# Performance work log

Hardware: AMD Instinct MI355X
Metric: run time of the kernel (lower is better)

Reference implementation:

```python
import jax, jax.numpy as jnp
import numpy as np

BN_EPS = 1e-5

def _bn_train(h, gamma, beta):
    # BatchNorm1d in training mode: batch statistics over the node dim
    mean = jnp.mean(h, axis=0)
    var = jnp.mean((h - mean) ** 2, axis=0)  # biased variance, as torch BN uses for normalization
    return gamma * (h - mean) * jax.lax.rsqrt(var + BN_EPS) + beta


def setup_inputs() -> dict:
    key = jax.random.key(0)
    ks = jax.random.split(key, 8)
    N, E = 100000, 1250000
    d_in, d_out = 64, 128
    x = jax.random.normal(ks[0], (N, d_in), dtype=jnp.float32)
    edge_index = jax.random.randint(ks[1], (2, E), 0, N, dtype=jnp.int64)
    s1 = 1.0 / np.sqrt(d_in)
    s2 = 1.0 / np.sqrt(d_out)
    W1 = jax.random.uniform(ks[2], (d_in, d_out), dtype=jnp.float32, minval=-s1, maxval=s1)
    b1 = jax.random.uniform(ks[3], (d_out,), dtype=jnp.float32, minval=-s1, maxval=s1)
    g1 = jnp.ones((d_out,), dtype=jnp.float32)
    be1 = jnp.zeros((d_out,), dtype=jnp.float32)
    W2 = jax.random.uniform(ks[4], (d_out, d_out), dtype=jnp.float32, minval=-s2, maxval=s2)
    b2 = jax.random.uniform(ks[5], (d_out,), dtype=jnp.float32, minval=-s2, maxval=s2)
    g2 = jnp.ones((d_out,), dtype=jnp.float32)
    be2 = jnp.zeros((d_out,), dtype=jnp.float32)
    return {"x": x, "edge_index": edge_index, "W1": W1, "b1": b1, "g1": g1, "be1": be1,
            "W2": W2, "b2": b2, "g2": g2, "be2": be2}


def reference(x, edge_index, W1, b1, g1, be1, W2, b2, g2, be2):
    src = edge_index[0]
    dst = edge_index[1]
    N = x.shape[0]
    # GIN aggregation: sum of neighbor features scattered to destination nodes
    agg = jax.ops.segment_sum(x[src], dst, num_segments=N)
    h = x + agg  # (1 + eps) * x + agg with eps = 0 (GINConv default)
    # MLP: Linear -> ReLU -> BN -> Linear -> ReLU -> BN
    h = jnp.maximum(h @ W1 + b1, 0.0)
    h = _bn_train(h, g1, be1)
    h = jnp.maximum(h @ W2 + b2, 0.0)
    h = _bn_train(h, g2, be2)
    return h
```

## Files before the change

kernel.cpp:

```cpp
#include <hip/hip_runtime.h>


#define NBMAX 512
#define CAP   8192
#define CPB   4096

__global__ __launch_bounds__(512) void k_zero(int* __restrict__ gcnt,
                                              float* __restrict__ stats)
{
    int t = threadIdx.x;
    gcnt[t] = 0;
    stats[t] = 0.f;
}

__global__ __launch_bounds__(256) void k_part(const int* __restrict__ ei, int E,
                                              int* __restrict__ gcnt,
                                              unsigned int* __restrict__ pk)
{
    __shared__ int cnt[NBMAX];
    __shared__ int gbase[NBMAX];
    const int tid = threadIdx.x;
    const int e0 = blockIdx.x * CPB;
    const int e1 = min(E, e0 + CPB);

    for (int i = tid; i < NBMAX; i += 256) cnt[i] = 0;
    __syncthreads();

    for (int e = e0 + tid; e < e1; e += 256)
        atomicAdd(&cnt[ei[E + e] >> 8], 1);
    __syncthreads();

    for (int i = tid; i < NBMAX; i += 256)
        gbase[i] = cnt[i] ? atomicAdd(&gcnt[i], cnt[i]) : 0;
    __syncthreads();
    for (int i = tid; i < NBMAX; i += 256) cnt[i] = 0;
    __syncthreads();

    for (int e = e0 + tid; e < e1; e += 256) {
        int dst = ei[E + e];
        int src = ei[e];
        int b = dst >> 8;
        int lr = atomicAdd(&cnt[b], 1);
        pk[(long)b * CAP + gbase[b] + lr] =
            ((unsigned)(dst & 255) << 17) | (unsigned)src;
    }
}

__global__ __launch_bounds__(256) void k_csr(const unsigned int* __restrict__ pk,
                                             const int* __restrict__ gcnt,
                                             int* __restrict__ nbr,
                                             int* __restrict__ beg,
                                             int* __restrict__ endq, int N)
{
    __shared__ int lcnt[256];
    __shared__ int lscan[256];
    const int tid = threadIdx.x;
    const int b = blockIdx.x;
    const int cnt = gcnt[b];
    const unsigned int* eb = pk + (long)b * CAP;

    lcnt[tid] = 0;
    __syncthreads();
    for (int j = tid; j < cnt; j += 256)
        atomicAdd(&lcnt[eb[j] >> 17], 1);
    __syncthreads();

    int v = lcnt[tid];
    lscan[tid] = v;
    __syncthreads();
    for (int off = 1; off < 256; off <<= 1) {
        int t = (tid >= off) ? lscan[tid - off] : 0;
        __syncthreads();
        lscan[tid] += t;
        __syncthreads();
    }
    int excl = lscan[tid] - v;

    int node = (b << 8) + tid;
    if (node < N) {
        beg[node]  = b * CAP + excl;
        endq[node] = b * CAP + excl + v;
    }
    lcnt[tid] = excl;
    __syncthreads();

    for (int j = tid; j < cnt; j += 256) {
        unsigned int p = eb[j];
        int lr = atomicAdd(&lcnt[p >> 17], 1);
        nbr[b * CAP + lr] = (int)(p & 0x1FFFFu);
    }
}

__global__ __launch_bounds__(256) void k_gather(const float4* __restrict__ x4,
                                                const int* __restrict__ beg,
                                                const int* __restrict__ endq,
                                                const int* __restrict__ nbr,
                                                float4* __restrict__ h04, int N)
{
    int wid  = threadIdx.x >> 6;
    int lane = threadIdx.x & 63;
    int node = blockIdx.x * 4 + wid;
    if (node >= N) return;
    int d4 = lane & 15;
    int g  = lane >> 4;
    int b = beg[node], e = endq[node];

    float4 acc = make_float4(0.f, 0.f, 0.f, 0.f);
    if (g == 0) acc = x4[(long)node * 16 + d4];

    for (int j = b + g; j < e; j += 4) {
        int s = nbr[j];
        float4 v = x4[(long)s * 16 + d4];
        acc.x += v.x; acc.y += v.y; acc.z += v.z; acc.w += v.w;
    }

#pragma unroll
    for (int m = 16; m <= 32; m <<= 1) {
        acc.x += __shfl_xor(acc.x, m, 64);
        acc.y += __shfl_xor(acc.y, m, 64);
        acc.z += __shfl_xor(acc.z, m, 64);
        acc.w += __shfl_xor(acc.w, m, 64);
    }

    if (g == 0) h04[(long)node * 16 + d4] = acc;
}

template<int K>
__global__ __launch_bounds__(256) void k_gemm_bias_relu(
    const float* __restrict__ A, const float* __restrict__ W,
    const float* __restrict__ bias, float* __restrict__ Out, int N,
    float* __restrict__ sums, float* __restrict__ sqs)
{
    __shared__ float sA[64][68];
    __shared__ float sW[64][128];
    __shared__ float lsum[128], lsq[128];

    const int tid = threadIdx.x;
    const int tx = tid & 15;
    const int ty = tid >> 4;
    const int row0 = blockIdx.x * 64;

    if (tid < 128) { lsum[tid] = 0.f; lsq[tid] = 0.f; }

    float acc[4][8];
#pragma unroll
    for (int i = 0; i < 4; ++i)
#pragma unroll
        for (int j = 0; j < 8; ++j) acc[i][j] = 0.f;

    for (int k0 = 0; k0 < K; k0 += 64) {
#pragma unroll
        for (int ch = 0; ch < 4; ++ch) {
            int idx = ch * 256 + tid;
            int r = idx >> 4, kq = idx & 15;
            int grow = row0 + r;
            float4 v = make_float4(0.f, 0.f, 0.f, 0.f);
            if (grow < N) v = *(const float4*)(A + (long)grow * K + (k0 + kq * 4));
            *(float4*)(&sA[r][kq * 4]) = v;
        }
#pragma unroll
        for (int ch = 0; ch < 8; ++ch) {
            int idx = ch * 256 + tid;
            int kr = idx >> 5, cq = idx & 31;
            *(float4*)(&sW[kr][cq * 4]) = *(const float4*)(W + (long)(k0 + kr) * 128 + cq * 4);
        }
        __syncthreads();

#pragma unroll 4
        for (int k4 = 0; k4 < 16; ++k4) {
            float4 a0 = *(const float4*)(&sA[ty * 4 + 0][k4 * 4]);
            float4 a1 = *(const float4*)(&sA[ty * 4 + 1][k4 * 4]);
            float4 a2 = *(const float4*)(&sA[ty * 4 + 2][k4 * 4]);
            float4 a3 = *(const float4*)(&sA[ty * 4 + 3][k4 * 4]);
            float ar[4][4] = {{a0.x, a0.y, a0.z, a0.w},
                              {a1.x, a1.y, a1.z, a1.w},
                              {a2.x, a2.y, a2.z, a2.w},
                              {a3.x, a3.y, a3.z, a3.w}};
#pragma unroll
            for (int kk = 0; kk < 4; ++kk) {
                int k = k4 * 4 + kk;
                float4 w0 = *(const float4*)(&sW[k][tx * 4]);
                float4 w1 = *(const float4*)(&sW[k][64 + tx * 4]);
                float w[8] = {w0.x, w0.y, w0.z, w0.w, w1.x, w1.y, w1.z, w1.w};
#pragma unroll
                for (int i = 0; i < 4; ++i)
#pragma unroll
                    for (int j = 0; j < 8; ++j)
                        acc[i][j] = fmaf(ar[i][kk], w[j], acc[i][j]);
            }
        }
        __syncthreads();
    }

    float b[8];
#pragma unroll
    for (int j = 0; j < 4; ++j) b[j] = bias[tx * 4 + j];
#pragma unroll
    for (int j = 0; j < 4; ++j) b[4 + j] = bias[64 + tx * 4 + j];

    float s[8], q[8];
#pragma unroll
    for (int j = 0; j < 8; ++j) { s[j] = 0.f; q[j] = 0.f; }

#pragma unroll
    for (int i = 0; i < 4; ++i) {
        int grow = row0 + ty * 4 + i;
        if (grow < N) {
            float o[8];
#pragma unroll
            for (int j = 0; j < 8; ++j) {
                o[j] = fmaxf(acc[i][j] + b[j], 0.f);
                s[j] += o[j];
                q[j] = fmaf(o[j], o[j], q[j]);
            }
            float4 o0 = make_float4(o[0], o[1], o[2], o[3]);
            float4 o1 = make_float4(o[4], o[5], o[6], o[7]);
            *(float4*)(Out + (long)grow * 128 + tx * 4)      = o0;
            *(float4*)(Out + (long)grow * 128 + 64 + tx * 4) = o1;
        }
    }

#pragma unroll
    for (int j = 0; j < 8; ++j) {
        s[j] += __shfl_xor(s[j], 16, 64);
        s[j] += __shfl_xor(s[j], 32, 64);
        q[j] += __shfl_xor(q[j], 16, 64);
        q[j] += __shfl_xor(q[j], 32, 64);
    }
    if ((tid & 63) < 16) {
#pragma unroll
        for (int j = 0; j < 4; ++j) {
            atomicAdd(&lsum[tx * 4 + j],      s[j]);
            atomicAdd(&lsq [tx * 4 + j],      q[j]);
            atomicAdd(&lsum[64 + tx * 4 + j], s[4 + j]);
            atomicAdd(&lsq [64 + tx * 4 + j], q[4 + j]);
        }
    }
    __syncthreads();
    if (tid < 128) {
        atomicAdd(&sums[tid], lsum[tid]);
        atomicAdd(&sqs[tid],  lsq[tid]);
    }
}

__global__ void k_bn_fold(const float* __restrict__ stats,
                          const float* __restrict__ gamma, const float* __restrict__ beta,
                          const float* __restrict__ W2, const float* __restrict__ b2,
                          float* __restrict__ W2p, float* __restrict__ b2p, float invN)
{
    __shared__ float as[128], cs[128];
    int j = threadIdx.x;
    float m = stats[j] * invN;
    float v = stats[128 + j] * invN - m * m;
    float a = gamma[j] * rsqrtf(v + 1e-5f);
    float c = beta[j] - m * a;
    as[j] = a;
    cs[j] = c;
    __syncthreads();
    float bb = b2[j];
    for (int k = 0; k < 128; ++k) {
        float w = W2[k * 128 + j];
        W2p[k * 128 + j] = as[k] * w;
        bb = fmaf(cs[k], w, bb);
    }
    b2p[j] = bb;
}

__global__ void k_bn_coeffs(const float* __restrict__ stats,
                            const float* __restrict__ gamma, const float* __restrict__ beta,
                            float* __restrict__ ac, float invN)
{
    int j = threadIdx.x;
    float m = stats[j] * invN;
    float v = stats[128 + j] * invN - m * m;
    float a = gamma[j] * rsqrtf(v + 1e-5f);
    ac[j] = a;
    ac[128 + j] = beta[j] - m * a;
}

__global__ __launch_bounds__(256) void k_bn_apply(float* __restrict__ out,
                                                  const float* __restrict__ ac, long n4)
{
    __shared__ float sa[128], sc[128];
    if (threadIdx.x < 128) {
        sa[threadIdx.x] = ac[threadIdx.x];
        sc[threadIdx.x] = ac[128 + threadIdx.x];
    }
    __syncthreads();
    long i = (long)blockIdx.x * 256 + threadIdx.x;
    if (i < n4) {
        float4 v = ((float4*)out)[i];
        int c0 = (int)((i * 4) & 127);
        v.x = fmaf(v.x, sa[c0 + 0], sc[c0 + 0]);
        v.y = fmaf(v.y, sa[c0 + 1], sc[c0 + 1]);
        v.z = fmaf(v.z, sa[c0 + 2], sc[c0 + 2]);
        v.w = fmaf(v.w, sa[c0 + 3], sc[c0 + 3]);
        ((float4*)out)[i] = v;
    }
}

extern "C" void kernel_launch(void* const* d_in, const int* in_sizes, int n_in,
                              void* d_out, int out_size, void* d_ws, size_t ws_size,
                              hipStream_t stream)
{
    const float* x   = (const float*)d_in[0];
    const int*   ei  = (const int*)  d_in[1];
    const float* W1  = (const float*)d_in[2];
    const float* b1  = (const float*)d_in[3];
    const float* g1  = (const float*)d_in[4];
    const float* be1 = (const float*)d_in[5];
    const float* W2  = (const float*)d_in[6];
    const float* b2  = (const float*)d_in[7];
    const float* g2  = (const float*)d_in[8];
    const float* be2 = (const float*)d_in[9];
    float* out = (float*)d_out;

    const int N = in_sizes[0] / 64;
    const int E = in_sizes[1] / 2;
    const int nbuckets = (N + 255) >> 8;

    float* ws    = (float*)d_ws;
    float* h0    = ws;
    float* h1    = h0 + (long)N * 64;
    float* W2p   = h1 + (long)N * 128;
    float* b2p   = W2p + 128 * 128;
    float* stats = b2p + 128;
    float* ac    = stats + 512;
    int*   gcnt  = (int*)(ac + 256);

    unsigned int* pk  = (unsigned int*)h1;
    int*          nbr = (int*)h1 + (long)NBMAX * CAP;
    int*          beg = nbr + (long)NBMAX * CAP;
    int*          endq = beg + N;

    const float invN = 1.0f / (float)N;

    k_zero<<<1, 512, 0, stream>>>(gcnt, stats);

    k_part<<<(E + CPB - 1) / CPB, 256, 0, stream>>>(ei, E, gcnt, pk);

    k_csr<<<nbuckets, 256, 0, stream>>>(pk, gcnt, nbr, beg, endq, N);

    k_gather<<<(N + 3) / 4, 256, 0, stream>>>((const float4*)x, beg, endq, nbr,
                                              (float4*)h0, N);

    int gBlocks = (N + 63) / 64;
    k_gemm_bias_relu<64><<<gBlocks, 256, 0, stream>>>(h0, W1, b1, h1, N,
                                                      stats, stats + 128);

    k_bn_fold<<<1, 128, 0, stream>>>(stats, g1, be1, W2, b2, W2p, b2p, invN);

    k_gemm_bias_relu<128><<<gBlocks, 256, 0, stream>>>(h1, W2p, b2p, out, N,
                                                       stats + 256, stats + 384);

    k_bn_coeffs<<<1, 128, 0, stream>>>(stats + 256, g2, be2, ac, invN);

    long n4o = (long)N * 128 / 4;
    k_bn_apply<<<(int)((n4o + 255) / 256), 256, 0, stream>>>(out, ac, n4o);
}
```

Before: 330.3 us.

## Replace FP32 SIMT GEMMs with split-bf16 MFMA GEMMs

Both dense layers now run on bf16 MFMA instructions instead of scalar FP32 FMAs. Operands are split into high and low bf16 parts, and three MFMAs per tile approximate FP32 accuracy. Weights are pre-split and transposed by a small prep kernel and by the BN-fold kernel. Tiles grow to 128 rows per block. The cost is extra conversion work in the A-tile load, scalar (non-vector) output stores, and a small loss of precision from dropping the low-low product.

```diff
diff --git a/kernel.cpp b/kernel.cpp
--- a/kernel.cpp
+++ b/kernel.cpp
@@ -1,9 +1,31 @@
 #include <hip/hip_runtime.h>
 
+
+typedef unsigned short u16;
+typedef unsigned int   u32;
+typedef __attribute__((ext_vector_type(8))) short  s8v;
+typedef __attribute__((ext_vector_type(4))) float  f4v;
 
 #define NBMAX 512
 #define CAP   8192
 #define CPB   4096
+
+__device__ __forceinline__ u16 f2bf(float f) {
+    u32 u = __builtin_bit_cast(u32, f);
+    return (u16)((u + 0x7FFFu + ((u >> 16) & 1u)) >> 16);
+}
+__device__ __forceinline__ float bf2f(u16 h) {
+    u32 u = ((u32)h) << 16;
+    return __builtin_bit_cast(float, u);
+}
+__device__ __forceinline__ uint4 pk8(const u16* p) {
+    uint4 r;
+    r.x = (u32)p[0] | ((u32)p[1] << 16);
+    r.y = (u32)p[2] | ((u32)p[3] << 16);
+    r.z = (u32)p[4] | ((u32)p[5] << 16);
+    r.w = (u32)p[6] | ((u32)p[7] << 16);
+    return r;
+}
 
 __global__ __launch_bounds__(512) void k_zero(int* __restrict__ gcnt,
                                               float* __restrict__ stats)
@@ -125,115 +147,129 @@
     if (g == 0) h04[(long)node * 16 + d4] = acc;
 }
 
+__global__ void k_wprep(const float* __restrict__ W1,
+                        u16* __restrict__ w1th, u16* __restrict__ w1tl)
+{
+    int j = threadIdx.x;
+    for (int k = 0; k < 64; ++k) {
+        float w = W1[k * 128 + j];
+        u16 h = f2bf(w);
+        w1th[j * 64 + k] = h;
+        w1tl[j * 64 + k] = f2bf(w - bf2f(h));
+    }
+}
+
 template<int K>
-__global__ __launch_bounds__(256) void k_gemm_bias_relu(
-    const float* __restrict__ A, const float* __restrict__ W,
-    const float* __restrict__ bias, float* __restrict__ Out, int N,
+__global__ __launch_bounds__(256) void k_gemm_mfma(
+    const float* __restrict__ A, const u16* __restrict__ WTh,
+    const u16* __restrict__ WTl, const float* __restrict__ bias,
+    float* __restrict__ Out, int N,
     float* __restrict__ sums, float* __restrict__ sqs)
 {
-    __shared__ float sA[64][68];
-    __shared__ float sW[64][128];
+    __shared__ u16 sAh[128][40], sAl[128][40];
+    __shared__ u16 sBh[128][40], sBl[128][40];
     __shared__ float lsum[128], lsq[128];
 
-    const int tid = threadIdx.x;
-    const int tx = tid & 15;
-    const int ty = tid >> 4;
-    const int row0 = blockIdx.x * 64;
+    const int tid  = threadIdx.x;
+    const int lane = tid & 63, wid = tid >> 6;
+    const int wr = wid >> 1, wc = wid & 1;
+    const int cq = lane & 15, rq = lane >> 4;
+    const int koff = rq * 8;
+    const int row0 = blockIdx.x * 128;
+    const int sr = tid >> 1;
+    const int hf = tid & 1;
 
     if (tid < 128) { lsum[tid] = 0.f; lsq[tid] = 0.f; }
 
-    float acc[4][8];
+    f4v acc[4][4];
 #pragma unroll
     for (int i = 0; i < 4; ++i)
 #pragma unroll
-        for (int j = 0; j < 8; ++j) acc[i][j] = 0.f;
-
-    for (int k0 = 0; k0 < K; k0 += 64) {
-#pragma unroll
-        for (int ch = 0; ch < 4; ++ch) {
-            int idx = ch * 256 + tid;
-            int r = idx >> 4, kq = idx & 15;
-            int grow = row0 + r;
-            float4 v = make_float4(0.f, 0.f, 0.f, 0.f);
-            if (grow < N) v = *(const float4*)(A + (long)grow * K + (k0 + kq * 4));
-            *(float4*)(&sA[r][kq * 4]) = v;
-        }
-#pragma unroll
-        for (int ch = 0; ch < 8; ++ch) {
-            int idx = ch * 256 + tid;
-            int kr = idx >> 5, cq = idx & 31;
-            *(float4*)(&sW[kr][cq * 4]) = *(const float4*)(W + (long)(k0 + kr) * 128 + cq * 4);
-        }
+        for (int j = 0; j < 4; ++j)
+#pragma unroll
+            for (int e = 0; e < 4; ++e) acc[i][j][e] = 0.f;
+
+    for (int k0 = 0; k0 < K; k0 += 32) {
         __syncthreads();
-
-#pragma unroll 4
-        for (int k4 = 0; k4 < 16; ++k4) {
-            float4 a0 = *(const float4*)(&sA[ty * 4 + 0][k4 * 4]);
-            float4 a1 = *(const float4*)(&sA[ty * 4 + 1][k4 * 4]);
-            float4 a2 = *(const float4*)(&sA[ty * 4 + 2][k4 * 4]);
-            float4 a3 = *(const float4*)(&sA[ty * 4 + 3][k4 * 4]);
-            float ar[4][4] = {{a0.x, a0.y, a0.z, a0.w},
-                              {a1.x, a1.y, a1.z, a1.w},
-                              {a2.x, a2.y, a2.z, a2.w},
-                              {a3.x, a3.y, a3.z, a3.w}};
-#pragma unroll
-            for (int kk = 0; kk < 4; ++kk) {
-                int k = k4 * 4 + kk;
-                float4 w0 = *(const float4*)(&sW[k][tx * 4]);
-                float4 w1 = *(const float4*)(&sW[k][64 + tx * 4]);
-                float w[8] = {w0.x, w0.y, w0.z, w0.w, w1.x, w1.y, w1.z, w1.w};
-#pragma unroll
-                for (int i = 0; i < 4; ++i)
-#pragma unroll
-                    for (int j = 0; j < 8; ++j)
-                        acc[i][j] = fmaf(ar[i][kk], w[j], acc[i][j]);
+        {
+            float v[16];
+            int grow = row0 + sr;
+            if (grow < N) {
+                const float4* src = (const float4*)(A + (long)grow * K + k0 + hf * 16);
+#pragma unroll
+                for (int i = 0; i < 4; ++i) {
+                    float4 f = src[i];
+                    v[4*i] = f.x; v[4*i+1] = f.y; v[4*i+2] = f.z; v[4*i+3] = f.w;
+                }
+            } else {
+#pragma unroll
+                for (int i = 0; i < 16; ++i) v[i] = 0.f;
             }
+            u16 hh[16], ll[16];
+#pragma unroll
+            for (int i = 0; i < 16; ++i) {
+                hh[i] = f2bf(v[i]);
+                ll[i] = f2bf(v[i] - bf2f(hh[i]));
+            }
+            *(uint4*)&sAh[sr][hf*16]     = pk8(hh);
+            *(uint4*)&sAh[sr][hf*16 + 8] = pk8(hh + 8);
+            *(uint4*)&sAl[sr][hf*16]     = pk8(ll);
+            *(uint4*)&sAl[sr][hf*16 + 8] = pk8(ll + 8);
+        }
+        {
+            const uint4* sh = (const uint4*)(WTh + (long)sr * K + k0 + hf * 16);
+            const uint4* sl = (const uint4*)(WTl + (long)sr * K + k0 + hf * 16);
+            *(uint4*)&sBh[sr][hf*16]     = sh[0];
+            *(uint4*)&sBh[sr][hf*16 + 8] = sh[1];
+            *(uint4*)&sBl[sr][hf*16]     = sl[0];
+            *(uint4*)&sBl[sr][hf*16 + 8] = sl[1];
         }
         __syncthreads();
-    }
-
-    float b[8];
-#pragma unroll
-    for (int j = 0; j < 4; ++j) b[j] = bias[tx * 4 + j];
-#pragma unroll
-    for (int j = 0; j < 4; ++j) b[4 + j] = bias[64 + tx * 4 + j];
-
-    float s[8], q[8];
-#pragma unroll
-    for (int j = 0; j < 8; ++j) { s[j] = 0.f; q[j] = 0.f; }
-
-#pragma unroll
-    for (int i = 0; i < 4; ++i) {
-        int grow = row0 + ty * 4 + i;
-        if (grow < N) {
-            float o[8];
-#pragma unroll
-            for (int j = 0; j < 8; ++j) {
-                o[j] = fmaxf(acc[i][j] + b[j], 0.f);
-                s[j] += o[j];
-                q[j] = fmaf(o[j], o[j], q[j]);
+
+        s8v ah[4], al[4];
+#pragma unroll
+        for (int tr = 0; tr < 4; ++tr) {
+            int rr = wr * 64 + tr * 16 + cq;
+            ah[tr] = __builtin_bit_cast(s8v, *(const uint4*)&sAh[rr][koff]);
+            al[tr] = __builtin_bit_cast(s8v, *(const uint4*)&sAl[rr][koff]);
+        }
+#pragma unroll
+        for (int tc = 0; tc < 4; ++tc) {
+            int cc = wc * 64 + tc * 16 + cq;
+            s8v bh = __builtin_bit_cast(s8v, *(const uint4*)&sBh[cc][koff]);
+            s8v bl = __builtin_bit_cast(s8v, *(const uint4*)&sBl[cc][koff]);
+#pragma unroll
+            for (int tr = 0; tr < 4; ++tr) {
+                acc[tr][tc] = __builtin_amdgcn_mfma_f32_16x16x32_bf16(ah[tr], bh, acc[tr][tc], 0, 0, 0);
+                acc[tr][tc] = __builtin_amdgcn_mfma_f32_16x16x32_bf16(al[tr], bh, acc[tr][tc], 0, 0, 0);
+                acc[tr][tc] = __builtin_amdgcn_mfma_f32_16x16x32_bf16(ah[tr], bl, acc[tr][tc], 0, 0, 0);
             }
-            float4 o0 = make_float4(o[0], o[1], o[2], o[3]);
-            float4 o1 = make_float4(o[4], o[5], o[6], o[7]);
-            *(float4*)(Out + (long)grow * 128 + tx * 4)      = o0;
-            *(float4*)(Out + (long)grow * 128 + 64 + tx * 4) = o1;
-        }
-    }
-
-#pragma unroll
-    for (int j = 0; j < 8; ++j) {
-        s[j] += __shfl_xor(s[j], 16, 64);
-        s[j] += __shfl_xor(s[j], 32, 64);
-        q[j] += __shfl_xor(q[j], 16, 64);
-        q[j] += __shfl_xor(q[j], 32, 64);
-    }
-    if ((tid & 63) < 16) {
-#pragma unroll
-        for (int j = 0; j < 4; ++j) {
-            atomicAdd(&lsum[tx * 4 + j],      s[j]);
-            atomicAdd(&lsq [tx * 4 + j],      q[j]);
-            atomicAdd(&lsum[64 + tx * 4 + j], s[4 + j]);
-            atomicAdd(&lsq [64 + tx * 4 + j], q[4 + j]);
+        }
+    }
+
+#pragma unroll
+    for (int tc = 0; tc < 4; ++tc) {
+        int col = wc * 64 + tc * 16 + cq;
+        float b = bias[col];
+        float s = 0.f, q = 0.f;
+#pragma unroll
+        for (int tr = 0; tr < 4; ++tr) {
+#pragma unroll
+            for (int e = 0; e < 4; ++e) {
+                int row = row0 + wr * 64 + tr * 16 + rq * 4 + e;
+                if (row < N) {
+                    float o = fmaxf(acc[tr][tc][e] + b, 0.f);
+                    Out[(long)row * 128 + col] = o;
+                    s += o;
+                    q = fmaf(o, o, q);
+                }
+            }
+        }
+        s += __shfl_xor(s, 16, 64); s += __shfl_xor(s, 32, 64);
+        q += __shfl_xor(q, 16, 64); q += __shfl_xor(q, 32, 64);
+        if (lane < 16) {
+            atomicAdd(&lsum[col], s);
+            atomicAdd(&lsq[col],  q);
         }
     }
     __syncthreads();
@@ -246,7 +282,8 @@
 __global__ void k_bn_fold(const float* __restrict__ stats,
                           const float* __restrict__ gamma, const float* __restrict__ beta,
                           const float* __restrict__ W2, const float* __restrict__ b2,
-                          float* __restrict__ W2p, float* __restrict__ b2p, float invN)
+                          u16* __restrict__ w2th, u16* __restrict__ w2tl,
+                          float* __restrict__ b2p, float invN)
 {
     __shared__ float as[128], cs[128];
     int j = threadIdx.x;
@@ -259,8 +296,11 @@
     __syncthreads();
     float bb = b2[j];
     for (int k = 0; k < 128; ++k) {
-        float w = W2[k * 128 + j];
-        W2p[k * 128 + j] = as[k] * w;
+        float w  = W2[k * 128 + j];
+        float wp = as[k] * w;
+        u16 h = f2bf(wp);
+        w2th[j * 128 + k] = h;
+        w2tl[j * 128 + k] = f2bf(wp - bf2f(h));
         bb = fmaf(cs[k], w, bb);
     }
     b2p[j] = bb;
@@ -322,20 +362,25 @@
     float* ws    = (float*)d_ws;
     float* h0    = ws;
     float* h1    = h0 + (long)N * 64;
-    float* W2p   = h1 + (long)N * 128;
-    float* b2p   = W2p + 128 * 128;
+    float* b2p   = h1 + (long)N * 128;
     float* stats = b2p + 128;
     float* ac    = stats + 512;
     int*   gcnt  = (int*)(ac + 256);
-
-    unsigned int* pk  = (unsigned int*)h1;
-    int*          nbr = (int*)h1 + (long)NBMAX * CAP;
-    int*          beg = nbr + (long)NBMAX * CAP;
+    u16*   w1th  = (u16*)(gcnt + NBMAX);
+    u16*   w1tl  = w1th + 128 * 64;
+    u16*   w2th  = w1tl + 128 * 64;
+    u16*   w2tl  = w2th + 128 * 128;
+
+    unsigned int* pk   = (unsigned int*)h1;
+    int*          nbr  = (int*)h1 + (long)NBMAX * CAP;
+    int*          beg  = nbr + (long)NBMAX * CAP;
     int*          endq = beg + N;
 
     const float invN = 1.0f / (float)N;
 
     k_zero<<<1, 512, 0, stream>>>(gcnt, stats);
+
+    k_wprep<<<1, 128, 0, stream>>>(W1, w1th, w1tl);
 
     k_part<<<(E + CPB - 1) / CPB, 256, 0, stream>>>(ei, E, gcnt, pk);
 
@@ -344,14 +389,15 @@
     k_gather<<<(N + 3) / 4, 256, 0, stream>>>((const float4*)x, beg, endq, nbr,
                                               (float4*)h0, N);
 
-    int gBlocks = (N + 63) / 64;
-    k_gemm_bias_relu<64><<<gBlocks, 256, 0, stream>>>(h0, W1, b1, h1, N,
-                                                      stats, stats + 128);
-
-    k_bn_fold<<<1, 128, 0, stream>>>(stats, g1, be1, W2, b2, W2p, b2p, invN);
-
-    k_gemm_bias_relu<128><<<gBlocks, 256, 0, stream>>>(h1, W2p, b2p, out, N,
-                                                       stats + 256, stats + 384);
+    int gB = (N + 127) / 128;
+    k_gemm_mfma<64><<<gB, 256, 0, stream>>>(h0, w1th, w1tl, b1, h1, N,
+                                            stats, stats + 128);
+
+    k_bn_fold<<<1, 128, 0, stream>>>(stats, g1, be1, W2, b2, w2th, w2tl,
+                                     b2p, invN);
+
+    k_gemm_mfma<128><<<gB, 256, 0, stream>>>(h1, w2th, w2tl, b2p, out, N,
+                                             stats + 256, stats + 384);
 
     k_bn_coeffs<<<1, 128, 0, stream>>>(stats + 256, g2, be2, ac, invN);
 
```

Measured after the change: 321.4 us. 2.7% less time.
